# Optimization experiments

Measured on AMD Instinct MI355X. Metric: run time of the kernel, lower is better.

## Reference

```python
import jax, jax.numpy as jnp
import numpy as np

L, B, D, H, P = 4096, 4, 1024, 16, 256
HD = D // H
EPS = 1e-5


def _layer_norm(x, g, b):
    m = jnp.mean(x, axis=-1, keepdims=True)
    v = jnp.mean(jnp.square(x - m), axis=-1, keepdims=True)
    return (x - m) / jnp.sqrt(v + EPS) * g + b


def setup_inputs() -> dict:
    key = jax.random.key(0)
    ks = jax.random.split(key, 8)
    w = lambda k, shape: jax.random.normal(k, shape, jnp.float32) * 0.02
    return {
        "query": jax.random.normal(ks[0], (L, B, D), jnp.float32),
        "q_w": w(ks[1], (D, D)), "q_b": jnp.zeros((D,), jnp.float32),
        "k_w": w(ks[2], (D, D)), "k_b": jnp.zeros((D,), jnp.float32),
        "v_w": w(ks[3], (D, D)), "v_b": jnp.zeros((D,), jnp.float32),
        "e_weight": w(ks[4], (1, H, P, HD)),
        "e_out_w": w(ks[5], (D, D)), "e_out_b": jnp.zeros((D,), jnp.float32),
        "ln_g": jnp.ones((D,), jnp.float32), "ln_b": jnp.zeros((D,), jnp.float32),
        "out_w": w(ks[6], (D, D)), "out_b": jnp.zeros((D,), jnp.float32),
    }


def reference(query, q_w, q_b, k_w, k_b, v_w, v_b, e_weight,
              e_out_w, e_out_b, ln_g, ln_b, out_w, out_b):
    scaling = HD ** -0.5
    # ---- _compute_kv (kv_same=True, no padding mask) ----
    # kv: (L,B,D) -> (B,H,HD,L)
    kvh = query.reshape(L, B, H, HD).transpose(1, 2, 3, 0)
    # pkv = relu(E @ (kv * scaling)) : (B,H,P,L)
    pkv = jax.nn.relu(jnp.einsum('hpd,bhdl->bhpl', e_weight[0], kvh * scaling))
    # kv = pkv @ kv^T : (B,H,P,HD)
    kv = jnp.einsum('bhpl,bhdl->bhpd', pkv, kvh)
    # -> (P,B,D), e_out linear, residual add of e_weight, layer norm
    kv = kv.transpose(2, 0, 1, 3).reshape(P, B, D)
    kv = kv @ e_out_w.T + e_out_b
    kv = kv.reshape(P, B, H, HD) + e_weight.transpose(2, 0, 1, 3)  # broadcast (P,1,H,HD)
    kv = _layer_norm(kv.reshape(P, B, D), ln_g, ln_b)  # (P,B,D)

    # ---- standard MHA against the compressed kv ----
    q = (query @ q_w.T + q_b) * scaling            # (L,B,D)
    k = kv @ k_w.T + k_b                           # (P,B,D)
    v = kv @ v_w.T + v_b                           # (P,B,D)
    qh = q.reshape(L, B, H, HD)
    kh = k.reshape(P, B, H, HD)
    vh = v.reshape(P, B, H, HD)
    logits = jnp.einsum('lbhd,pbhd->bhlp', qh, kh)
    probs = jax.nn.softmax(logits, axis=-1)
    attn = jnp.einsum('bhlp,pbhd->lbhd', probs, vh).reshape(L, B, D)
    return attn @ out_w.T + out_b
```

## Files before the change

### kernel.cpp

```cpp
#include <hip/hip_runtime.h>
#include <hip/hip_bf16.h>
#include <cstdint>
#include <cstddef>

#define LL 4096
#define BB 4
#define DD 1024
#define HH 16
#define PP 256
#define HDD 64
#define LC 8
#define LCHUNK 512

constexpr float kScaling = 0.125f;
constexpr float kEps = 1e-5f;

typedef __attribute__((ext_vector_type(8))) short bf16x8;
typedef __attribute__((ext_vector_type(4))) short short4v;
typedef __attribute__((ext_vector_type(4))) float f32x4;

#define MFMA16(a, b, c) __builtin_amdgcn_mfma_f32_16x16x32_bf16((a), (b), (c), 0, 0, 0)

__device__ __forceinline__ unsigned short f2bf(float f) {
  unsigned int u = __builtin_bit_cast(unsigned int, f);
  u += 0x7FFFu + ((u >> 16) & 1u);
  return (unsigned short)(u >> 16);
}
__device__ __forceinline__ unsigned int f2bf2(float lo, float hi) {
  __hip_bfloat162 h = __float22bfloat162_rn(make_float2(lo, hi));
  unsigned int u;
  __builtin_memcpy(&u, &h, 4);
  return u;
}
__device__ __forceinline__ float bf2f(unsigned short u) {
  return __builtin_bit_cast(float, ((unsigned int)u) << 16);
}

__device__ __forceinline__ void gll16(const void* g, void* l) {
  __builtin_amdgcn_global_load_lds(
      (const __attribute__((address_space(1))) unsigned int*)g,
      (__attribute__((address_space(3))) unsigned int*)l, 16, 0, 0);
}

__global__ __launch_bounds__(256) void k_cvt_w(
    const float* __restrict__ w0, const float* __restrict__ w1,
    const float* __restrict__ w2, const float* __restrict__ w3,
    const float* __restrict__ w4, const float* __restrict__ w5,
    unsigned short* __restrict__ d0, unsigned short* __restrict__ d1,
    unsigned short* __restrict__ d2, unsigned short* __restrict__ d3,
    unsigned short* __restrict__ d4, unsigned short* __restrict__ d5) {
  int i = blockIdx.x * 256 + threadIdx.x;
  int w = i >> 17, off = i & 131071;
  const float* src; unsigned short* dst;
  if (w == 0) { src = w0; dst = d0; }
  else if (w == 1) { src = w1; dst = d1; }
  else if (w == 2) { src = w2; dst = d2; }
  else if (w == 3) { src = w3; dst = d3; }
  else if (w == 4) { src = w4; dst = d4; }
  else { if (off >= 32768) return; src = w5; dst = d5; }
  const float4* s = (const float4*)(src + (size_t)off * 8);
  float4 a = s[0], b = s[1];
  uint4 o;
  o.x = f2bf2(a.x, a.y); o.y = f2bf2(a.z, a.w);
  o.z = f2bf2(b.x, b.y); o.w = f2bf2(b.z, b.w);
  *(uint4*)(dst + (size_t)off * 8) = o;
}

__global__ __launch_bounds__(256) void k_compress_mfma(
    const float* __restrict__ q32, const unsigned short* __restrict__ ewbf,
    unsigned short* __restrict__ qbf_out, unsigned short* __restrict__ parts) {
  const int bh = blockIdx.x, lc = blockIdx.y;
  const int b = bh >> 4, h = bh & 15;
  const int tid = threadIdx.x, wv = tid >> 6, lane = tid & 63;
  const int fr = lane & 15, fg = lane >> 4;

  __shared__ __align__(16) char Xf[16384];
  __shared__ __align__(16) char Xl[8192];
  __shared__ __align__(16) char Xtl[8192];
  __shared__ __align__(16) char Pl[32768];

  bf16x8 ef[4][2];
#pragma unroll
  for (int pt = 0; pt < 4; ++pt)
#pragma unroll
    for (int kc = 0; kc < 2; ++kc)
      ef[pt][kc] = *(const bf16x8*)(ewbf +
          (size_t)((h * PP + wv * 64 + pt * 16 + fr) * HDD) + kc * 32 + fg * 8);

  f32x4 acc[4][4];
#pragma unroll
  for (int i = 0; i < 4; ++i)
#pragma unroll
    for (int j = 0; j < 4; ++j) acc[i][j] = (f32x4){0.f, 0.f, 0.f, 0.f};

  const int l0 = lc * LCHUNK;

  auto stageX = [&](int t) {
#pragma unroll
    for (int j = 0; j < 4; ++j) {
      int u = tid + j * 256;
      int l = u >> 4, h16 = u & 15;
      int col = 8 * ((h16 >> 1) ^ ((l >> 1) & 7)) + (h16 & 1) * 4;
      gll16(q32 + ((size_t)(l0 + t * 64 + l) * BB + b) * DD + h * HDD + col,
            Xf + u * 16);
    }
  };

  stageX(0);
  __syncthreads();

  for (int t = 0; t < LCHUNK / 64; ++t) {
    {
      int l2 = tid >> 3, c8 = tid & 7;
      int l = 2 * l2;
      int slot = ((c8 ^ (l2 & 7)) << 5);
      float4 a0 = *(const float4*)(Xf + l * 256 + slot);
      float4 a1 = *(const float4*)(Xf + l * 256 + slot + 16);
      float4 b0 = *(const float4*)(Xf + (l + 1) * 256 + slot);
      float4 b1 = *(const float4*)(Xf + (l + 1) * 256 + slot + 16);
      size_t rowbase = ((size_t)(l0 + t * 64 + l) * BB + b) * DD + h * HDD + c8 * 8;
      unsigned int W[4], U[4];
      W[0] = f2bf2(a0.x, a0.y); W[1] = f2bf2(a0.z, a0.w);
      W[2] = f2bf2(a1.x, a1.y); W[3] = f2bf2(a1.z, a1.w);
      U[0] = f2bf2(b0.x, b0.y); U[1] = f2bf2(b0.z, b0.w);
      U[2] = f2bf2(b1.x, b1.y); U[3] = f2bf2(b1.z, b1.w);
      uint4 V0 = {W[0], W[1], W[2], W[3]};
      uint4 V1 = {U[0], U[1], U[2], U[3]};
      *(uint4*)(qbf_out + rowbase) = V0;
      *(uint4*)(qbf_out + rowbase + BB * DD) = V1;
      *(uint4*)(Xl + l * 128 + ((c8 ^ (l & 7)) << 4)) = V0;
      *(uint4*)(Xl + (l + 1) * 128 + ((c8 ^ ((l + 1) & 7)) << 4)) = V1;
#pragma unroll
      for (int j = 0; j < 4; ++j) {
        int dd0 = c8 * 8 + 2 * j, dd1 = dd0 + 1;
        unsigned int pe = (W[j] & 0xFFFFu) | (U[j] << 16);
        unsigned int po = (W[j] >> 16) | (U[j] & 0xFFFF0000u);
        *(unsigned int*)(Xtl + dd0 * 128 +
            ((((l >> 3) ^ (dd0 & 7) ^ (dd0 >> 3)) & 7) << 4) + ((l & 7) << 1)) = pe;
        *(unsigned int*)(Xtl + dd1 * 128 +
            ((((l >> 3) ^ (dd1 & 7) ^ (dd1 >> 3)) & 7) << 4) + ((l & 7) << 1)) = po;
      }
    }
    __syncthreads();
    if (t + 1 < LCHUNK / 64) stageX(t + 1);

#pragma unroll
    for (int lt = 0; lt < 4; ++lt) {
      int rl = lt * 16 + fr;
      bf16x8 xa0 = *(const bf16x8*)(Xl + rl * 128 + (((0 + fg) ^ (rl & 7)) << 4));
      bf16x8 xa1 = *(const bf16x8*)(Xl + rl * 128 + (((4 + fg) ^ (rl & 7)) << 4));
#pragma unroll
      for (int pt = 0; pt < 4; ++pt) {
        f32x4 s = (f32x4){0.f, 0.f, 0.f, 0.f};
        s = MFMA16(xa0, ef[pt][0], s);
        s = MFMA16(xa1, ef[pt][1], s);
        uint2 pk2;
        pk2.x = f2bf2(fmaxf(s[0] * kScaling, 0.f), fmaxf(s[1] * kScaling, 0.f));
        pk2.y = f2bf2(fmaxf(s[2] * kScaling, 0.f), fmaxf(s[3] * kScaling, 0.f));
        int p = wv * 64 + pt * 16 + fr;
        int lbase = lt * 16 + fg * 4;
        int slot = lbase >> 3;
        *(uint2*)(Pl + p * 128 + ((slot ^ (p & 7)) << 4) + ((lbase & 7) << 1)) = pk2;
      }
    }
    asm volatile("s_waitcnt lgkmcnt(0)" ::: "memory");
    __builtin_amdgcn_sched_barrier(0);
#pragma unroll
    for (int kc = 0; kc < 2; ++kc) {
      bf16x8 pa[4], xb[4];
#pragma unroll
      for (int pt = 0; pt < 4; ++pt) {
        int p = wv * 64 + pt * 16 + fr;
        pa[pt] = *(const bf16x8*)(Pl + p * 128 + (((kc * 4 + fg) ^ (p & 7)) << 4));
      }
#pragma unroll
      for (int dt = 0; dt < 4; ++dt) {
        int dd = dt * 16 + fr;
        xb[dt] = *(const bf16x8*)(Xtl + dd * 128 +
                  ((((kc * 4 + fg) ^ (dd & 7) ^ (dd >> 3)) & 7) << 4));
      }
#pragma unroll
      for (int pt = 0; pt < 4; ++pt)
#pragma unroll
        for (int dt = 0; dt < 4; ++dt)
          acc[pt][dt] = MFMA16(pa[pt], xb[dt], acc[pt][dt]);
    }
    __syncthreads();
  }
  unsigned short* op = parts + (size_t)(lc * 64 + bh) * PP * HDD;
#pragma unroll
  for (int pt = 0; pt < 4; ++pt)
#pragma unroll
    for (int dt = 0; dt < 4; ++dt)
#pragma unroll
      for (int r = 0; r < 4; ++r) {
        int p = wv * 64 + pt * 16 + fg * 4 + r;
        int dd = dt * 16 + fr;
        op[(size_t)p * HDD + dd] = f2bf(acc[pt][dt][r]);
      }
}

__global__ __launch_bounds__(256) void k_reduce(const unsigned short* __restrict__ parts,
                                                unsigned short* __restrict__ kv_raw_bf) {
  int u = blockIdx.x * 256 + threadIdx.x;
  size_t off = (size_t)u * 8;
  float s[8] = {0.f, 0.f, 0.f, 0.f, 0.f, 0.f, 0.f, 0.f};
#pragma unroll
  for (int lcc = 0; lcc < LC; ++lcc) {
    bf16x8 v = *(const bf16x8*)(parts + (size_t)lcc * (64 * PP * HDD) + off);
#pragma unroll
    for (int j = 0; j < 8; ++j) s[j] += bf2f((unsigned short)v[j]);
  }
  int i = (int)off;
  int d = i & 63, p = (i >> 6) & 255, bh = i >> 14;
  int b = bh >> 4, h = bh & 15;
  uint4 o;
  o.x = f2bf2(s[0], s[1]); o.y = f2bf2(s[2], s[3]);
  o.z = f2bf2(s[4], s[5]); o.w = f2bf2(s[6], s[7]);
  *(uint4*)(kv_raw_bf + (size_t)(p * BB + b) * DD + h * HDD + d) = o;
}

template <int MODE, typename OUTT>
__device__ __forceinline__ void gemm_body(
    const unsigned short* __restrict__ A, const unsigned short* __restrict__ W,
    const float* __restrict__ bias, const float* __restrict__ ew,
    OUTT* __restrict__ C, int m0, int n0, char* Al, char* Bl) {
  const int tid = threadIdx.x;
  const int wv = tid >> 6, lane = tid & 63;
  const int fr = lane & 15, fg = lane >> 4;
  const int wr = wv >> 1, wc = wv & 1;

  f32x4 acc[4][4];
#pragma unroll
  for (int i = 0; i < 4; ++i)
#pragma unroll
    for (int j = 0; j < 4; ++j) acc[i][j] = (f32x4){0.f, 0.f, 0.f, 0.f};

  for (int k0 = 0; k0 < DD; k0 += 64) {
    __syncthreads();
#pragma unroll
    for (int j = 0; j < 4; ++j) {
      int u = tid + j * 256;
      int row = u >> 3, slot = u & 7;
      size_t gcol = (size_t)(k0 + 8 * (slot ^ (row & 7)));
      gll16(A + (size_t)(m0 + row) * DD + gcol, Al + u * 16);
      gll16(W + (size_t)(n0 + row) * DD + gcol, Bl + u * 16);
    }
    __syncthreads();
#pragma unroll
    for (int kc = 0; kc < 2; ++kc) {
      bf16x8 af[4], bfr[4];
#pragma unroll
      for (int mt = 0; mt < 4; ++mt) {
        int r = wr * 64 + mt * 16 + fr;
        af[mt] = *(const bf16x8*)(Al + r * 128 + (((kc * 4 + fg) ^ (r & 7)) << 4));
      }
#pragma unroll
      for (int nt = 0; nt < 4; ++nt) {
        int r = wc * 64 + nt * 16 + fr;
        bfr[nt] = *(const bf16x8*)(Bl + r * 128 + (((kc * 4 + fg) ^ (r & 7)) << 4));
      }
#pragma unroll
      for (int mt = 0; mt < 4; ++mt)
#pragma unroll
        for (int nt = 0; nt < 4; ++nt)
          acc[mt][nt] = MFMA16(af[mt], bfr[nt], acc[mt][nt]);
    }
  }

  float bs[4];
#pragma unroll
  for (int nt = 0; nt < 4; ++nt) bs[nt] = bias[n0 + wc * 64 + nt * 16 + fr];
#pragma unroll
  for (int mt = 0; mt < 4; ++mt)
#pragma unroll
    for (int nt = 0; nt < 4; ++nt) {
      int n = n0 + wc * 64 + nt * 16 + fr;
#pragma unroll
      for (int r = 0; r < 4; ++r) {
        int m = m0 + wr * 64 + mt * 16 + fg * 4 + r;
        float v = acc[mt][nt][r] + bs[nt];
        if (MODE == 1) v *= kScaling;
        if (MODE == 2) {
          int p = m >> 2, hh = n >> 6, d2 = n & 63;
          v += ew[(size_t)((hh << 8) + p) * HDD + d2];
        }
        if constexpr (sizeof(OUTT) == 2)
          C[(size_t)m * DD + n] = (OUTT)f2bf(v);
        else
          C[(size_t)m * DD + n] = v;
      }
    }
}

template <int MODE, typename OUTT>
__global__ __launch_bounds__(256) void k_gemm_mfma(
    const unsigned short* __restrict__ A, const unsigned short* __restrict__ W,
    const float* __restrict__ bias, const float* __restrict__ ew,
    OUTT* __restrict__ C) {
  __shared__ __align__(16) char Al[16384];
  __shared__ __align__(16) char Bl[16384];
  gemm_body<MODE, OUTT>(A, W, bias, ew, C, blockIdx.x * 128, blockIdx.y * 128, Al, Bl);
}

__global__ __launch_bounds__(256) void k_gemm_kv(
    const unsigned short* __restrict__ A,
    const unsigned short* __restrict__ Wk, const unsigned short* __restrict__ Wv,
    const float* __restrict__ kb, const float* __restrict__ vb,
    unsigned short* __restrict__ Ck, unsigned short* __restrict__ Cv) {
  __shared__ __align__(16) char Al[16384];
  __shared__ __align__(16) char Bl[16384];
  if (blockIdx.z == 0)
    gemm_body<0, unsigned short>(A, Wk, kb, nullptr, Ck,
                                 blockIdx.x * 128, blockIdx.y * 128, Al, Bl);
  else
    gemm_body<0, unsigned short>(A, Wv, vb, nullptr, Cv,
                                 blockIdx.x * 128, blockIdx.y * 128, Al, Bl);
}

template <int MODE, typename OUTT>
__global__ __launch_bounds__(512, 2) void k_gemm256(
    const unsigned short* __restrict__ A, const unsigned short* __restrict__ W,
    const float* __restrict__ bias, OUTT* __restrict__ C) {
  __shared__ __align__(16) char lds[131072];
  const int tid = threadIdx.x;
  const int wv = tid >> 6, lane = tid & 63;
  const int fr = lane & 15, fg = lane >> 4;
  const int wm = wv >> 2, wn = wv & 3;
  const int m0 = blockIdx.x * 256, n0 = blockIdx.y * 256;
  const int srow = tid >> 2, sslot = tid & 3;

  auto stageHalf = [&](const unsigned short* __restrict__ G, int g0, int colbase,
                       int dstBase) {
#pragma unroll
    for (int j = 0; j < 2; ++j) {
      int row = srow + j * 128;
      int gs = sslot ^ ((row >> 1) & 3);
      gll16(G + (size_t)(g0 + row) * DD + colbase + gs * 8,
            lds + dstBase + (tid + j * 512) * 16);
    }
  };
  auto rdA = [&](int mf, int kc, int cb) -> bf16x8 {
    int r = wm * 128 + mf * 16 + fr;
    return *(const bf16x8*)(lds + cb + kc * 16384 + r * 64 +
                            ((fg ^ ((r >> 1) & 3)) << 4));
  };
  auto rdB = [&](int nf, int kc, int cb) -> bf16x8 {
    int r = wn * 64 + nf * 16 + fr;
    return *(const bf16x8*)(lds + cb + 32768 + kc * 16384 + r * 64 +
                            ((fg ^ ((r >> 1) & 3)) << 4));
  };

  f32x4 acc[8][4];
#pragma unroll
  for (int i = 0; i < 8; ++i)
#pragma unroll
    for (int j = 0; j < 4; ++j) acc[i][j] = (f32x4){0.f, 0.f, 0.f, 0.f};
  bf16x8 a[8], b[4];

  stageHalf(A, m0, 0, 0);
  stageHalf(W, n0, 0, 32768);
  stageHalf(A, m0, 32, 16384);
  stageHalf(W, n0, 32, 32768 + 16384);
  stageHalf(A, m0, 64, 65536);
  stageHalf(W, n0, 64, 65536 + 32768);
  asm volatile("s_waitcnt vmcnt(4)" ::: "memory");
  __builtin_amdgcn_s_barrier();

  const int NT = DD / 64;
  for (int t = 0; t < NT; ++t) {
    const int cb = (t & 1) << 16;
    const int nb = cb ^ 65536;
    const int k1 = (t + 1) * 64, k2 = (t + 2) * 64;

#pragma unroll
    for (int i = 0; i < 8; ++i) a[i] = rdA(i, 0, cb);
#pragma unroll
    for (int i = 0; i < 4; ++i) b[i] = rdB(i, 0, cb);
    if (t + 1 < NT) {
      stageHalf(A, m0, k1 + 32, nb + 16384);
      stageHalf(W, n0, k1 + 32, nb + 32768 + 16384);
    }
    asm volatile("s_waitcnt lgkmcnt(0)" ::: "memory");
    __builtin_amdgcn_sched_barrier(0);
    __builtin_amdgcn_s_setprio(1);
#pragma unroll
    for (int mf = 0; mf < 8; ++mf)
#pragma unroll
      for (int nf = 0; nf < 4; ++nf)
        acc[mf][nf] = MFMA16(a[mf], b[nf], acc[mf][nf]);
    __builtin_amdgcn_s_setprio(0);
    __builtin_amdgcn_s_barrier();

#pragma unroll
    for (int i = 0; i < 8; ++i) a[i] = rdA(i, 1, cb);
#pragma unroll
    for (int i = 0; i < 4; ++i) b[i] = rdB(i, 1, cb);
    if (t + 2 < NT) {
      stageHalf(A, m0, k2, cb);
      stageHalf(W, n0, k2, cb + 32768);
    }
    asm volatile("s_waitcnt lgkmcnt(0)" ::: "memory");
    __builtin_amdgcn_sched_barrier(0);
    __builtin_amdgcn_s_setprio(1);
#pragma unroll
    for (int mf = 0; mf < 8; ++mf)
#pragma unroll
      for (int nf = 0; nf < 4; ++nf)
        acc[mf][nf] = MFMA16(a[mf], b[nf], acc[mf][nf]);
    __builtin_amdgcn_s_setprio(0);
    if (t + 2 < NT) {
      asm volatile("s_waitcnt vmcnt(4)" ::: "memory");
    } else if (t + 1 < NT) {
      asm volatile("s_waitcnt vmcnt(0)" ::: "memory");
    }
    __builtin_amdgcn_s_barrier();
  }

  float bs[4];
#pragma unroll
  for (int nf = 0; nf < 4; ++nf) bs[nf] = bias[n0 + wn * 64 + nf * 16 + fr];
#pragma unroll
  for (int mf = 0; mf < 8; ++mf)
#pragma unroll
    for (int nf = 0; nf < 4; ++nf) {
      int n = n0 + wn * 64 + nf * 16 + fr;
#pragma unroll
      for (int r = 0; r < 4; ++r) {
        int m = m0 + wm * 128 + mf * 16 + fg * 4 + r;
        float v = acc[mf][nf][r] + bs[nf];
        if (MODE == 1) v *= kScaling;
        if constexpr (sizeof(OUTT) == 2)
          C[(size_t)m * DD + n] = (OUTT)f2bf(v);
        else
          C[(size_t)m * DD + n] = v;
      }
    }
}

__global__ __launch_bounds__(256) void k_ln(const float* __restrict__ x,
                                            const float* __restrict__ g,
                                            const float* __restrict__ bb,
                                            unsigned short* __restrict__ y) {
  const int r = blockIdx.x;
  const int tid = threadIdx.x;
  const float* xr = x + (size_t)r * DD;
  float4 v = *(const float4*)(xr + tid * 4);
  float s1 = v.x + v.y + v.z + v.w;
  float s2 = v.x * v.x + v.y * v.y + v.z * v.z + v.w * v.w;
#pragma unroll
  for (int off = 32; off > 0; off >>= 1) {
    s1 += __shfl_down(s1, off);
    s2 += __shfl_down(s2, off);
  }
  __shared__ float w1[4], w2[4];
  if ((tid & 63) == 0) { w1[tid >> 6] = s1; w2[tid >> 6] = s2; }
  __syncthreads();
  float S1 = w1[0] + w1[1] + w1[2] + w1[3];
  float S2 = w2[0] + w2[1] + w2[2] + w2[3];
  float mean = S1 * (1.f / DD);
  float var = S2 * (1.f / DD) - mean * mean;
  float rstd = rsqrtf(var + kEps);
  float4 gv = *(const float4*)(g + tid * 4);
  float4 bv = *(const float4*)(bb + tid * 4);
  uint2 o;
  o.x = f2bf2((v.x - mean) * rstd * gv.x + bv.x, (v.y - mean) * rstd * gv.y + bv.y);
  o.y = f2bf2((v.z - mean) * rstd * gv.z + bv.z, (v.w - mean) * rstd * gv.w + bv.w);
  *(uint2*)(y + (size_t)r * DD + tid * 4) = o;
}

__global__ __launch_bounds__(512, 2) void k_attn_mfma(
    const unsigned short* __restrict__ qbf, const unsigned short* __restrict__ kbf,
    const unsigned short* __restrict__ vbf, unsigned short* __restrict__ attn) {
  const int bh = blockIdx.y;
  const int b = bh >> 4, h = bh & 15;
  const int tid = threadIdx.x, wv = tid >> 6, lane = tid & 63;
  const int fr = lane & 15, fg = lane >> 4;
  const int bl0 = blockIdx.x * 128;

  __shared__ __align__(16) char Kl[16384];
  __shared__ __align__(16) char Vt[16384];
  __shared__ __align__(16) char Pl[32768];

  const size_t qrow = ((size_t)(bl0 + wv * 16 + fr) * BB + b) * DD + h * HDD;
  bf16x8 qf0 = *(const bf16x8*)(qbf + qrow + fg * 8);
  bf16x8 qf1 = *(const bf16x8*)(qbf + qrow + 32 + fg * 8);

  f32x4 o[4];
#pragma unroll
  for (int dt = 0; dt < 4; ++dt) o[dt] = (f32x4){0.f, 0.f, 0.f, 0.f};
  float psum = 0.f;
  char* Pw = Pl + wv * 4096;

  const int p2 = tid >> 3, c8v = tid & 7;
  const size_t vbase = ((size_t)((2 * p2) * BB + b)) * DD + h * HDD + c8v * 8;
  bf16x8 va = *(const bf16x8*)(vbf + vbase);
  bf16x8 vb_ = *(const bf16x8*)(vbf + vbase + BB * DD);

#pragma unroll
  for (int ph = 0; ph < 2; ++ph) {
    if (ph == 1) {
      asm volatile("s_waitcnt lgkmcnt(0)" ::: "memory");
      __builtin_amdgcn_s_barrier();
    }
#pragma unroll
    for (int j = 0; j < 2; ++j) {
      int u = tid + j * 512;
      int p = u >> 3, slot = u & 7;
      gll16(kbf + ((size_t)((ph * 128 + p) * BB + b)) * DD + h * HDD +
                8 * (slot ^ (p & 7)),
            Kl + u * 16);
    }
    {
      int pl = (2 * p2) & 63, pc = p2 >> 5;
      char* base = Vt + pc * 8192;
#pragma unroll
      for (int i = 0; i < 8; ++i) {
        int dd = c8v * 8 + i;
        unsigned int packed = (unsigned int)(unsigned short)va[i] |
                              ((unsigned int)(unsigned short)vb_[i] << 16);
        *(unsigned int*)(base + dd * 128 +
            ((((pl >> 3) ^ (dd & 7) ^ (dd >> 3)) & 7) << 4) + ((pl & 7) << 1)) = packed;
      }
    }
    bf16x8 van, vbn;
    if (ph == 0) {
      van = *(const bf16x8*)(vbf + vbase + (size_t)128 * BB * DD);
      vbn = *(const bf16x8*)(vbf + vbase + (size_t)129 * BB * DD);
    }
    asm volatile("s_waitcnt lgkmcnt(0)" ::: "memory");
    if (ph == 0) {
      asm volatile("s_waitcnt vmcnt(2)" ::: "memory");
    } else {
      asm volatile("s_waitcnt vmcnt(0)" ::: "memory");
    }
    __builtin_amdgcn_s_barrier();
    __builtin_amdgcn_sched_barrier(0);

    f32x4 s[8];
    __builtin_amdgcn_s_setprio(1);
#pragma unroll
    for (int pt = 0; pt < 8; ++pt) {
      int pr = pt * 16 + fr;
      bf16x8 a0 = *(const bf16x8*)(Kl + pr * 128 + ((fg ^ (pr & 7)) << 4));
      bf16x8 a1 = *(const bf16x8*)(Kl + pr * 128 + (((4 + fg) ^ (pr & 7)) << 4));
      f32x4 acc = (f32x4){0.f, 0.f, 0.f, 0.f};
      acc = MFMA16(a0, qf0, acc);
      acc = MFMA16(a1, qf1, acc);
      s[pt] = acc;
    }
    __builtin_amdgcn_s_setprio(0);

#pragma unroll
    for (int pt = 0; pt < 8; ++pt) {
      float e0 = __expf(s[pt][0]), e1 = __expf(s[pt][1]);
      float e2 = __expf(s[pt][2]), e3 = __expf(s[pt][3]);
      psum += (e0 + e1) + (e2 + e3);
      uint2 pk2;
      pk2.x = f2bf2(e0, e1);
      pk2.y = f2bf2(e2, e3);
      int pbyte = (pt * 16 + fg * 4) * 2;
      int slot = pbyte >> 4, rem = pbyte & 15;
      *(uint2*)(Pw + fr * 256 + ((slot ^ (fr & 7)) << 4) + rem) = pk2;
    }
    asm volatile("s_waitcnt lgkmcnt(0)" ::: "memory");
    __builtin_amdgcn_sched_barrier(0);

    __builtin_amdgcn_s_setprio(1);
#pragma unroll
    for (int kc = 0; kc < 4; ++kc) {
      int slot = kc * 4 + fg;
      bf16x8 pa = *(const bf16x8*)(Pw + fr * 256 + ((slot ^ (fr & 7)) << 4));
      int sl2 = (kc & 1) * 4 + fg;
#pragma unroll
      for (int dt = 0; dt < 4; ++dt) {
        int dd = dt * 16 + fr;
        bf16x8 vbr = *(const bf16x8*)(Vt + (kc >> 1) * 8192 + dd * 128 +
                     (((sl2 ^ (dd & 7) ^ (dd >> 3)) & 7) << 4));
        o[dt] = MFMA16(pa, vbr, o[dt]);
      }
    }
    __builtin_amdgcn_s_setprio(0);

    if (ph == 0) { va = van; vb_ = vbn; }
  }

  psum += __shfl_xor(psum, 16);
  psum += __shfl_xor(psum, 32);

#pragma unroll
  for (int r = 0; r < 4; ++r) {
    int lloc = fg * 4 + r;
    float inv = 1.f / __shfl(psum, lloc);
    unsigned short* op = attn +
        ((size_t)(bl0 + wv * 16 + lloc) * BB + b) * DD + h * HDD;
#pragma unroll
    for (int dt = 0; dt < 4; ++dt)
      op[dt * 16 + fr] = f2bf(o[dt][r] * inv);
  }
}

extern "C" void kernel_launch(void* const* d_in, const int* in_sizes, int n_in,
                              void* d_out, int out_size, void* d_ws, size_t ws_size,
                              hipStream_t stream) {
  const float* query   = (const float*)d_in[0];
  const float* q_w     = (const float*)d_in[1];
  const float* q_b     = (const float*)d_in[2];
  const float* k_w     = (const float*)d_in[3];
  const float* k_b     = (const float*)d_in[4];
  const float* v_w     = (const float*)d_in[5];
  const float* v_b     = (const float*)d_in[6];
  const float* e_weight= (const float*)d_in[7];
  const float* e_out_w = (const float*)d_in[8];
  const float* e_out_b = (const float*)d_in[9];
  const float* ln_g    = (const float*)d_in[10];
  const float* ln_b    = (const float*)d_in[11];
  const float* out_w   = (const float*)d_in[12];
  const float* out_b   = (const float*)d_in[13];
  float* out = (float*)d_out;

  char* w = (char*)d_ws;
  unsigned short* parts   = (unsigned short*)w;
  unsigned short* q_bf    = (unsigned short*)w;
  unsigned short* attn_bf = (unsigned short*)(w + (32u << 20));
  unsigned short* query_bf= (unsigned short*)(w + (64u << 20));
  unsigned short* kv_raw  = (unsigned short*)(w + (96u << 20));
  float* kv_eo            = (float*)(w + (98u << 20));
  unsigned short* kv_ln   = (unsigned short*)(w + (102u << 20));
  unsigned short* k_buf   = (unsigned short*)(w + (104u << 20));
  unsigned short* v_buf   = (unsigned short*)(w + (106u << 20));
  unsigned short* wq  = (unsigned short*)(w + (108u << 20));
  unsigned short* wk  = (unsigned short*)(w + (110u << 20));
  unsigned short* wv_ = (unsigned short*)(w + (112u << 20));
  unsigned short* weo = (unsigned short*)(w + (114u << 20));
  unsigned short* wo  = (unsigned short*)(w + (116u << 20));
  unsigned short* ewb = (unsigned short*)(w + (118u << 20));

  k_cvt_w<<<2688, 256, 0, stream>>>(q_w, k_w, v_w, e_out_w, out_w, e_weight,
                                    wq, wk, wv_, weo, wo, ewb);

  k_compress_mfma<<<dim3(64, LC), 256, 0, stream>>>(query, ewb, query_bf, parts);
  k_reduce<<<512, 256, 0, stream>>>(parts, kv_raw);
  k_gemm_mfma<2, float><<<dim3(8, 8), 256, 0, stream>>>(kv_raw, weo, e_out_b, e_weight, kv_eo);
  k_ln<<<PP * BB, 256, 0, stream>>>(kv_eo, ln_g, ln_b, kv_ln);
  k_gemm256<1, unsigned short><<<dim3(64, 4), 512, 0, stream>>>(query_bf, wq, q_b, q_bf);
  k_gemm_kv<<<dim3(8, 8, 2), 256, 0, stream>>>(kv_ln, wk, wv_, k_b, v_b, k_buf, v_buf);
  k_attn_mfma<<<dim3(32, 64), 512, 0, stream>>>(q_bf, k_buf, v_buf, attn_bf);
  k_gemm256<0, float><<<dim3(64, 4), 512, 0, stream>>>(attn_bf, wo, out_b, out);
}
```

Baseline: 198.9 us.

## Replace 256x256 BK64 GEMM with 128x256 BK32 tile for higher occupancy

The large Q-projection and output-projection GEMMs move from a 256x256 tile with K-step 64 and 128KB of LDS to a 128x256 tile with K-step 32 and 48KB of LDS, with launch bounds raised to 4 blocks per CU. The grid doubles to 512 blocks, which gives better CU coverage on a device with many CUs and more waves to hide latency. The pipeline is reworked into a single-phase double buffer with a barrier before restaging. In exchange, arithmetic intensity per tile drops and there are twice as many barriers per K.

```diff
diff --git a/kernel.cpp b/kernel.cpp
--- a/kernel.cpp
+++ b/kernel.cpp
@@ -319,98 +319,71 @@
 }
 
 template <int MODE, typename OUTT>
-__global__ __launch_bounds__(512, 2) void k_gemm256(
+__global__ __launch_bounds__(512, 4) void k_gemm_bk32(
     const unsigned short* __restrict__ A, const unsigned short* __restrict__ W,
     const float* __restrict__ bias, OUTT* __restrict__ C) {
-  __shared__ __align__(16) char lds[131072];
+  __shared__ __align__(16) char lds[49152];
   const int tid = threadIdx.x;
   const int wv = tid >> 6, lane = tid & 63;
   const int fr = lane & 15, fg = lane >> 4;
   const int wm = wv >> 2, wn = wv & 3;
-  const int m0 = blockIdx.x * 256, n0 = blockIdx.y * 256;
-  const int srow = tid >> 2, sslot = tid & 3;
-
-  auto stageHalf = [&](const unsigned short* __restrict__ G, int g0, int colbase,
-                       int dstBase) {
+  const int m0 = blockIdx.x * 128, n0 = blockIdx.y * 256;
+
+  auto stageA = [&](int t, int base) {
+    int row = tid >> 2, slot = tid & 3;
+    int gcol = t * 32 + 8 * (slot ^ ((row >> 1) & 3));
+    gll16(A + (size_t)(m0 + row) * DD + gcol, lds + base + tid * 16);
+  };
+  auto stageB = [&](int t, int base) {
 #pragma unroll
     for (int j = 0; j < 2; ++j) {
-      int row = srow + j * 128;
-      int gs = sslot ^ ((row >> 1) & 3);
-      gll16(G + (size_t)(g0 + row) * DD + colbase + gs * 8,
-            lds + dstBase + (tid + j * 512) * 16);
+      int u = tid + j * 512;
+      int row = u >> 2, slot = u & 3;
+      int gcol = t * 32 + 8 * (slot ^ ((row >> 1) & 3));
+      gll16(W + (size_t)(n0 + row) * DD + gcol, lds + base + 8192 + u * 16);
     }
   };
-  auto rdA = [&](int mf, int kc, int cb) -> bf16x8 {
-    int r = wm * 128 + mf * 16 + fr;
-    return *(const bf16x8*)(lds + cb + kc * 16384 + r * 64 +
-                            ((fg ^ ((r >> 1) & 3)) << 4));
+  auto rdA = [&](int mf, int cb) -> bf16x8 {
+    int r = wm * 64 + mf * 16 + fr;
+    return *(const bf16x8*)(lds + cb + r * 64 + ((fg ^ ((r >> 1) & 3)) << 4));
   };
-  auto rdB = [&](int nf, int kc, int cb) -> bf16x8 {
+  auto rdB = [&](int nf, int cb) -> bf16x8 {
     int r = wn * 64 + nf * 16 + fr;
-    return *(const bf16x8*)(lds + cb + 32768 + kc * 16384 + r * 64 +
-                            ((fg ^ ((r >> 1) & 3)) << 4));
+    return *(const bf16x8*)(lds + cb + 8192 + r * 64 + ((fg ^ ((r >> 1) & 3)) << 4));
   };
 
-  f32x4 acc[8][4];
-#pragma unroll
-  for (int i = 0; i < 8; ++i)
+  f32x4 acc[4][4];
+#pragma unroll
+  for (int i = 0; i < 4; ++i)
 #pragma unroll
     for (int j = 0; j < 4; ++j) acc[i][j] = (f32x4){0.f, 0.f, 0.f, 0.f};
-  bf16x8 a[8], b[4];
-
-  stageHalf(A, m0, 0, 0);
-  stageHalf(W, n0, 0, 32768);
-  stageHalf(A, m0, 32, 16384);
-  stageHalf(W, n0, 32, 32768 + 16384);
-  stageHalf(A, m0, 64, 65536);
-  stageHalf(W, n0, 64, 65536 + 32768);
-  asm volatile("s_waitcnt vmcnt(4)" ::: "memory");
+  bf16x8 a[4], b[4];
+
+  stageA(0, 0); stageB(0, 0);
+  stageA(1, 24576); stageB(1, 24576);
+  asm volatile("s_waitcnt vmcnt(3)" ::: "memory");
   __builtin_amdgcn_s_barrier();
 
-  const int NT = DD / 64;
+  const int NT = DD / 32;
   for (int t = 0; t < NT; ++t) {
-    const int cb = (t & 1) << 16;
-    const int nb = cb ^ 65536;
-    const int k1 = (t + 1) * 64, k2 = (t + 2) * 64;
-
-#pragma unroll
-    for (int i = 0; i < 8; ++i) a[i] = rdA(i, 0, cb);
-#pragma unroll
-    for (int i = 0; i < 4; ++i) b[i] = rdB(i, 0, cb);
-    if (t + 1 < NT) {
-      stageHalf(A, m0, k1 + 32, nb + 16384);
-      stageHalf(W, n0, k1 + 32, nb + 32768 + 16384);
-    }
+    const int cb = (t & 1) ? 24576 : 0;
+#pragma unroll
+    for (int i = 0; i < 4; ++i) a[i] = rdA(i, cb);
+#pragma unroll
+    for (int i = 0; i < 4; ++i) b[i] = rdB(i, cb);
     asm volatile("s_waitcnt lgkmcnt(0)" ::: "memory");
+    __builtin_amdgcn_s_barrier();
+    if (t + 2 < NT) { stageA(t + 2, cb); stageB(t + 2, cb); }
     __builtin_amdgcn_sched_barrier(0);
     __builtin_amdgcn_s_setprio(1);
 #pragma unroll
-    for (int mf = 0; mf < 8; ++mf)
-#pragma unroll
-      for (int nf = 0; nf < 4; ++nf)
-        acc[mf][nf] = MFMA16(a[mf], b[nf], acc[mf][nf]);
-    __builtin_amdgcn_s_setprio(0);
-    __builtin_amdgcn_s_barrier();
-
-#pragma unroll
-    for (int i = 0; i < 8; ++i) a[i] = rdA(i, 1, cb);
-#pragma unroll
-    for (int i = 0; i < 4; ++i) b[i] = rdB(i, 1, cb);
-    if (t + 2 < NT) {
-      stageHalf(A, m0, k2, cb);
-      stageHalf(W, n0, k2, cb + 32768);
-    }
-    asm volatile("s_waitcnt lgkmcnt(0)" ::: "memory");
-    __builtin_amdgcn_sched_barrier(0);
-    __builtin_amdgcn_s_setprio(1);
-#pragma unroll
-    for (int mf = 0; mf < 8; ++mf)
+    for (int mf = 0; mf < 4; ++mf)
 #pragma unroll
       for (int nf = 0; nf < 4; ++nf)
         acc[mf][nf] = MFMA16(a[mf], b[nf], acc[mf][nf]);
     __builtin_amdgcn_s_setprio(0);
     if (t + 2 < NT) {
-      asm volatile("s_waitcnt vmcnt(4)" ::: "memory");
+      asm volatile("s_waitcnt vmcnt(3)" ::: "memory");
     } else if (t + 1 < NT) {
       asm volatile("s_waitcnt vmcnt(0)" ::: "memory");
     }
@@ -421,13 +394,13 @@
 #pragma unroll
   for (int nf = 0; nf < 4; ++nf) bs[nf] = bias[n0 + wn * 64 + nf * 16 + fr];
 #pragma unroll
-  for (int mf = 0; mf < 8; ++mf)
+  for (int mf = 0; mf < 4; ++mf)
 #pragma unroll
     for (int nf = 0; nf < 4; ++nf) {
       int n = n0 + wn * 64 + nf * 16 + fr;
 #pragma unroll
       for (int r = 0; r < 4; ++r) {
-        int m = m0 + wm * 128 + mf * 16 + fg * 4 + r;
+        int m = m0 + wm * 64 + mf * 16 + fg * 4 + r;
         float v = acc[mf][nf][r] + bs[nf];
         if (MODE == 1) v *= kScaling;
         if constexpr (sizeof(OUTT) == 2)
@@ -643,8 +616,8 @@
   k_reduce<<<512, 256, 0, stream>>>(parts, kv_raw);
   k_gemm_mfma<2, float><<<dim3(8, 8), 256, 0, stream>>>(kv_raw, weo, e_out_b, e_weight, kv_eo);
   k_ln<<<PP * BB, 256, 0, stream>>>(kv_eo, ln_g, ln_b, kv_ln);
-  k_gemm256<1, unsigned short><<<dim3(64, 4), 512, 0, stream>>>(query_bf, wq, q_b, q_bf);
+  k_gemm_bk32<1, unsigned short><<<dim3(128, 4), 512, 0, stream>>>(query_bf, wq, q_b, q_bf);
   k_gemm_kv<<<dim3(8, 8, 2), 256, 0, stream>>>(kv_ln, wk, wv_, k_b, v_b, k_buf, v_buf);
   k_attn_mfma<<<dim3(32, 64), 512, 0, stream>>>(q_bf, k_buf, v_buf, attn_bf);
-  k_gemm256<0, float><<<dim3(64, 4), 512, 0, stream>>>(attn_bf, wo, out_b, out);
-}
+  k_gemm_bk32<0, float><<<dim3(128, 4), 512, 0, stream>>>(attn_bf, wo, out_b, out);
+}
```

Result: slower. 203.8 us (+2.5%).
